# Performance work log

Hardware: AMD Instinct MI355X
Metric: run time of the kernel (lower is better)

The kernel has to match this reference:

```python
import jax, jax.numpy as jnp
import numpy as np

TOP_K = 2
ALPHA = 1.702
LIMIT = 7.0


def setup_inputs() -> dict:
    key = jax.random.key(0)
    ks = jax.random.split(key, 7)
    B, S, H, I, E = 1, 2048, 1024, 1024, 8
    scale = 0.02
    return {
        "hidden_states": jax.random.normal(ks[0], (B, S, H), dtype=jnp.float32),
        "router_w": jax.random.normal(ks[1], (H, E), dtype=jnp.float32) * scale,
        "router_b": jax.random.normal(ks[2], (E,), dtype=jnp.float32) * scale,
        "gate_up_proj": jax.random.normal(ks[3], (E, H, 2 * I), dtype=jnp.float32) * scale,
        "gate_up_bias": jax.random.normal(ks[4], (E, 2 * I), dtype=jnp.float32) * scale,
        "down_proj": jax.random.normal(ks[5], (E, I, H), dtype=jnp.float32) * scale,
        "down_bias": jax.random.normal(ks[6], (E, H), dtype=jnp.float32) * scale,
    }


def reference(hidden_states, router_w, router_b, gate_up_proj, gate_up_bias, down_proj, down_bias):
    # hidden_states: [B, S, H]; gate_up_proj: [E, H, 2I]; down_proj: [E, I, H]
    E = gate_up_proj.shape[0]
    # --- router (GPT-OSS style): top-k logits, softmax over top-k, scatter to E slots ---
    logits = jnp.einsum("bsh,he->bse", hidden_states, router_w) + router_b  # [B,S,E]
    top_vals, top_idx = jax.lax.top_k(logits, TOP_K)                         # [B,S,K]
    topk_weights = jax.nn.softmax(top_vals, axis=-1)                         # [B,S,K]
    onehot = jax.nn.one_hot(top_idx, E, dtype=logits.dtype)                  # [B,S,K,E]
    router_scores = jnp.einsum("bsk,bske->bse", topk_weights, onehot)        # [B,S,E]
    # --- expert compute (dense over the small expert axis; selection via gather below,
    #     which matches the sparsity-masked grouped matmul + all_to_all_combine math) ---
    gu = jnp.einsum("bsh,ehf->bsef", hidden_states, gate_up_proj) + gate_up_bias  # [B,S,E,2I]
    gate = gu[..., 0::2]  # interleaved gate
    up = gu[..., 1::2]    # interleaved up
    gate = jnp.minimum(gate, LIMIT)
    up = jnp.maximum(jnp.minimum(up, LIMIT), -LIMIT)
    glu = gate * jax.nn.sigmoid(gate * ALPHA)
    activated = (up + 1.0) * glu                                             # [B,S,E,I]
    down = jnp.einsum("bsei,eih->bseh", activated, down_proj) + down_bias    # [B,S,E,H]
    # combine: gather each token's K selected expert outputs, weighted sum
    sel = jnp.take_along_axis(down, top_idx[..., None], axis=2)              # [B,S,K,H]
    output = jnp.einsum("bskh,bsk->bsh", sel, topk_weights)                  # [B,S,H]
    return output, router_scores
```

## Files before the change

### kernel.cpp

```cpp
#include <hip/hip_runtime.h>
#include <stdint.h>


#define Sd 2048
#define Hd 1024
#define Id 1024

typedef __bf16 bf16x8 __attribute__((ext_vector_type(8)));
typedef _Float16 f16x8 __attribute__((ext_vector_type(8)));
typedef float f32x4 __attribute__((ext_vector_type(4)));

__device__ __forceinline__ f32x4 mfma_bf16(bf16x8 a, bf16x8 b, f32x4 c) {
  return __builtin_amdgcn_mfma_f32_16x16x32_bf16(a, b, c, 0, 0, 0);
}

__device__ __forceinline__ void gload16(const __bf16* g, __bf16* l) {
  __builtin_amdgcn_global_load_lds(
      (const __attribute__((address_space(1))) unsigned int*)g,
      (__attribute__((address_space(3))) unsigned int*)l, 16, 0, 0);
}

__device__ __forceinline__ unsigned int packbf(float lo, float hi) {
  __bf16 a = (__bf16)lo, b = (__bf16)hi;
  return (unsigned int)__builtin_bit_cast(unsigned short, a) |
         ((unsigned int)__builtin_bit_cast(unsigned short, b) << 16);
}

__global__ __launch_bounds__(256) void k_router(
    const float* __restrict__ x, const float* __restrict__ rw,
    const float* __restrict__ rb, float* __restrict__ scores,
    float* __restrict__ topw, int* __restrict__ eid,
    __bf16* __restrict__ xb) {
  const int lane = threadIdx.x & 63;
  const int t = blockIdx.x * 4 + (threadIdx.x >> 6);
  float acc[8];
#pragma unroll
  for (int e = 0; e < 8; ++e) acc[e] = 0.f;
  const float* xr = x + (size_t)t * Hd;
  unsigned int* xbo = (unsigned int*)(xb + (size_t)t * Hd);
#pragma unroll
  for (int j = 0; j < 8; ++j) {
    int h = j * 128 + lane * 2;
    float2 xv = *(const float2*)(xr + h);
    xbo[h >> 1] = packbf(xv.x, xv.y);
    const float4* wp = (const float4*)(rw + h * 8);
    float4 a0 = wp[0], a1 = wp[1], b0 = wp[2], b1 = wp[3];
    acc[0] += xv.x * a0.x; acc[1] += xv.x * a0.y;
    acc[2] += xv.x * a0.z; acc[3] += xv.x * a0.w;
    acc[4] += xv.x * a1.x; acc[5] += xv.x * a1.y;
    acc[6] += xv.x * a1.z; acc[7] += xv.x * a1.w;
    acc[0] += xv.y * b0.x; acc[1] += xv.y * b0.y;
    acc[2] += xv.y * b0.z; acc[3] += xv.y * b0.w;
    acc[4] += xv.y * b1.x; acc[5] += xv.y * b1.y;
    acc[6] += xv.y * b1.z; acc[7] += xv.y * b1.w;
  }
#pragma unroll
  for (int m = 32; m >= 1; m >>= 1) {
#pragma unroll
    for (int e = 0; e < 8; ++e) acc[e] += __shfl_xor(acc[e], m, 64);
  }
  if (lane == 0) {
    float lg[8];
#pragma unroll
    for (int e = 0; e < 8; ++e) lg[e] = acc[e] + rb[e];
    int i0 = 0; float v0 = lg[0];
#pragma unroll
    for (int e = 1; e < 8; ++e) if (lg[e] > v0) { v0 = lg[e]; i0 = e; }
    int i1 = -1; float v1 = -3.4e38f;
#pragma unroll
    for (int e = 0; e < 8; ++e) if (e != i0 && lg[e] > v1) { v1 = lg[e]; i1 = e; }
    float e1 = __expf(v1 - v0);
    float s = 1.f + e1;
    float w0 = 1.f / s, w1v = e1 / s;
#pragma unroll
    for (int e = 0; e < 8; ++e)
      scores[t * 8 + e] = (e == i0) ? w0 : ((e == i1) ? w1v : 0.f);
    topw[t * 2] = w0;
    topw[t * 2 + 1] = w1v;
    eid[t] = i0 | (i1 << 4);
  }
}

__global__ __launch_bounds__(256) void k_assign(
    const int* __restrict__ eid, int* __restrict__ cnt,
    int* __restrict__ assign, int* __restrict__ tokmap) {
  __shared__ int lcnt[8];
  const int tid = threadIdx.x;
  if (tid < 8) lcnt[tid] = 0;
  __syncthreads();
  for (int t = tid; t < 2048; t += 256) {
    int v = eid[t];
    int i0 = v & 15, i1 = v >> 4;
    int s0 = atomicAdd(&lcnt[i0], 1);
    assign[i0 * 2048 + s0] = t * 2;
    tokmap[t * 2] = (i0 << 11) | s0;
    int s1 = atomicAdd(&lcnt[i1], 1);
    assign[i1 * 2048 + s1] = t * 2 + 1;
    tokmap[t * 2 + 1] = (i1 << 11) | s1;
  }
  __syncthreads();
  if (tid < 8) cnt[tid] = lcnt[tid];
}

__global__ __launch_bounds__(256) void k_gather(
    const __bf16* __restrict__ xb, const int* __restrict__ cnt,
    const int* __restrict__ assign, __bf16* __restrict__ xg) {
  const int u = blockIdx.x;
  int acc = 0, myE = -1, myU0 = 0, nE = 0;
#pragma unroll
  for (int q = 0; q < 8; ++q) {
    int units = ((cnt[q] + 255) >> 8) * 16;
    if (u >= acc && u < acc + units) { myE = q; myU0 = acc; nE = cnt[q]; }
    acc += units;
  }
  if (myE < 0) return;
  const int lane = threadIdx.x & 63;
  const int wv = threadIdx.x >> 6;
  const int row = lane & 15, koff = (lane >> 4) * 8;
  const int slot = (u - myU0) * 16 + row;
  const bool valid = slot < nE;
  int tok = 0;
  if (valid) tok = assign[myE * 2048 + slot] >> 1;
  const __bf16* src = xb + (size_t)tok * Hd + koff;
#pragma unroll
  for (int s = 0; s < 8; ++s) {
    int k32 = wv + 4 * s;
    bf16x8 v;
#pragma unroll
    for (int j = 0; j < 8; ++j) v[j] = (__bf16)0.f;
    if (valid) v = *(const bf16x8*)(src + k32 * 32);
    *(bf16x8*)(xg + (((size_t)u * 32 + k32) * 64 + lane) * 8) = v;
  }
}

__global__ __launch_bounds__(256) void k_pre1(const float* __restrict__ wgu,
                                              __bf16* __restrict__ w1f) {
  const int b = blockIdx.x;
  const int nt = b & 7, kt = (b >> 3) & 15, e = b >> 7;
  __shared__ unsigned int Ls[16][16][34];
  const int tid = threadIdx.x;
  const int w = tid >> 6, lane = tid & 63;
  const float* src = wgu + (size_t)e * (1024 * 2048) +
                     (size_t)(kt * 64 + w * 16) * 2048 + nt * 256;
  const int i0 = lane * 2;
  const int c0 = i0 & 15, u0 = (i0 >> 4) * 2;
  const int c1 = (i0 + 1) & 15, u1 = ((i0 + 1) >> 4) * 2;
#pragma unroll
  for (int rp = 0; rp < 8; ++rp) {
    float4 fa = *(const float4*)(src + (size_t)(rp * 2) * 2048 + lane * 4);
    float4 fb = *(const float4*)(src + (size_t)(rp * 2 + 1) * 2048 + lane * 4);
    int r = w * 8 + rp;
    Ls[u0][c0][r] = packbf(fa.x, fb.x);
    Ls[u0 + 1][c0][r] = packbf(fa.y, fb.y);
    Ls[u1][c1][r] = packbf(fa.z, fb.z);
    Ls[u1 + 1][c1][r] = packbf(fa.w, fb.w);
  }
  __syncthreads();
  const int khi = lane >> 4, c = lane & 15;
#pragma unroll
  for (int uu = 0; uu < 8; ++uu) {
    int ul = w * 8 + uu, vu = ul >> 1, k32l = ul & 1;
    const unsigned int* p = &Ls[vu][c][k32l * 16 + khi * 4];
    uint2 q0 = *(const uint2*)p;
    uint2 q1 = *(const uint2*)(p + 2);
    int itg = nt * 8 + (vu >> 1), vf = vu & 1;
    size_t row = ((size_t)(e * 64 + itg) * 2 + vf) * 32 + (kt * 2 + k32l);
    uint4 o = {q0.x, q0.y, q1.x, q1.y};
    *(uint4*)(w1f + row * 512 + lane * 8) = o;
  }
}

__global__ __launch_bounds__(256) void k_pre2(const float* __restrict__ wdn,
                                              __bf16* __restrict__ w2f) {
  const int b = blockIdx.x;
  const int nt = b & 3, kt = (b >> 2) & 15, e = b >> 6;
  __shared__ unsigned int Ls[16][16][34];
  const int tid = threadIdx.x;
  const int w = tid >> 6, lane = tid & 63;
  const float* src = wdn + (size_t)e * (1024 * 1024) +
                     (size_t)(kt * 64 + w * 16) * 1024 + nt * 256;
#pragma unroll
  for (int rp = 0; rp < 8; ++rp) {
    float4 fa = *(const float4*)(src + (size_t)(rp * 2) * 1024 + lane * 4);
    float4 fb = *(const float4*)(src + (size_t)(rp * 2 + 1) * 1024 + lane * 4);
    int r = w * 8 + rp;
    float va[4] = {fa.x, fa.y, fa.z, fa.w};
    float vb[4] = {fb.x, fb.y, fb.z, fb.w};
#pragma unroll
    for (int q = 0; q < 4; ++q) {
      int cl = lane * 4 + q;
      Ls[cl >> 4][cl & 15][r] = packbf(va[q], vb[q]);
    }
  }
  __syncthreads();
  const int khi = lane >> 4, c = lane & 15;
#pragma unroll
  for (int uu = 0; uu < 8; ++uu) {
    int ul = w * 8 + uu, Fl = ul >> 1, k32l = ul & 1;
    const unsigned int* p = &Ls[Fl][c][k32l * 16 + khi * 4];
    uint2 q0 = *(const uint2*)p;
    uint2 q1 = *(const uint2*)(p + 2);
    size_t row = (size_t)(e * 64 + nt * 16 + Fl) * 32 + (kt * 2 + k32l);
    uint4 o = {q0.x, q0.y, q1.x, q1.y};
    *(uint4*)(w2f + row * 512 + lane * 8) = o;
  }
}

__global__ __launch_bounds__(512, 4) void k_gemm1(
    const __bf16* __restrict__ xg, const __bf16* __restrict__ w1f,
    const float* __restrict__ gub, const int* __restrict__ cnt,
    __bf16* __restrict__ abuf) {
  const int e = blockIdx.x & 7;
  const int it = blockIdx.x >> 3;
  const int n = cnt[e];
  if (n <= 0) return;
  __shared__ __align__(16) __bf16 Bs[2][32][512];
  __shared__ __align__(16) __bf16 Ts[256][16];
  const int tid = threadIdx.x;
  const int lane = tid & 63;
  const int wv = tid >> 6;

  const __bf16* wbase = w1f + (size_t)((e * 64 + it) * 2) * (32 * 512);
  __bf16* bsf = &Bs[0][0][0];
#pragma unroll
  for (int s = 0; s < 8; ++s) {
    int idx = s * 512 + tid;
    gload16(wbase + (size_t)idx * 8, bsf + (size_t)idx * 8);
  }
  const int iCol = it * 16 + (lane & 15);
  const float bg = gub[e * 2048 + 2 * iCol];
  const float bu = gub[e * 2048 + 2 * iCol + 1];
  int eb = 0;
#pragma unroll
  for (int q = 0; q < 8; ++q) eb += (q < e) ? (((cnt[q] + 255) >> 8) << 8) : 0;
  const int u0 = eb >> 4;
  const int nmt = (n + 255) >> 8;

  for (int mt = 0; mt < nmt; ++mt) {
    __syncthreads();
    const __bf16* ap0 =
        xg + ((size_t)(u0 + mt * 16 + 2 * wv) * 32) * 512 + lane * 8;
    const __bf16* ap1 = ap0 + (size_t)32 * 512;
    f32x4 acc[2][2];
#pragma unroll
    for (int a = 0; a < 2; ++a)
#pragma unroll
      for (int b = 0; b < 2; ++b) acc[a][b] = (f32x4){0.f, 0.f, 0.f, 0.f};
    bf16x8 pf[4][2];
#pragma unroll
    for (int d = 0; d < 4; ++d) {
      pf[d][0] = *(const bf16x8*)(ap0 + d * 512);
      pf[d][1] = *(const bf16x8*)(ap1 + d * 512);
    }
#pragma unroll 4
    for (int ks = 0; ks < 28; ++ks) {
      bf16x8 b0 = *(const bf16x8*)&Bs[0][ks][lane * 8];
      bf16x8 b1 = *(const bf16x8*)&Bs[1][ks][lane * 8];
      acc[0][0] = mfma_bf16(pf[ks & 3][0], b0, acc[0][0]);
      acc[0][1] = mfma_bf16(pf[ks & 3][0], b1, acc[0][1]);
      acc[1][0] = mfma_bf16(pf[ks & 3][1], b0, acc[1][0]);
      acc[1][1] = mfma_bf16(pf[ks & 3][1], b1, acc[1][1]);
      pf[ks & 3][0] = *(const bf16x8*)(ap0 + (ks + 4) * 512);
      pf[ks & 3][1] = *(const bf16x8*)(ap1 + (ks + 4) * 512);
    }
#pragma unroll
    for (int ks = 28; ks < 32; ++ks) {
      bf16x8 b0 = *(const bf16x8*)&Bs[0][ks][lane * 8];
      bf16x8 b1 = *(const bf16x8*)&Bs[1][ks][lane * 8];
      acc[0][0] = mfma_bf16(pf[ks & 3][0], b0, acc[0][0]);
      acc[0][1] = mfma_bf16(pf[ks & 3][0], b1, acc[0][1]);
      acc[1][0] = mfma_bf16(pf[ks & 3][1], b0, acc[1][0]);
      acc[1][1] = mfma_bf16(pf[ks & 3][1], b1, acc[1][1]);
    }
#pragma unroll
    for (int mi = 0; mi < 2; ++mi) {
#pragma unroll
      for (int rr = 0; rr < 4; ++rr) {
        int row = wv * 32 + mi * 16 + (lane >> 4) * 4 + rr;
        float g = fminf(acc[mi][0][rr] + bg, 7.f);
        float u = fminf(fmaxf(acc[mi][1][rr] + bu, -7.f), 7.f);
        float sg = 1.f / (1.f + __expf(-1.702f * g));
        Ts[row][lane & 15] = (__bf16)((u + 1.f) * (g * sg));
      }
    }
    __syncthreads();
    {
      int r = tid & 15, hl = (tid >> 4) & 1, sbl = tid >> 5;
      bf16x8 v = *(const bf16x8*)&Ts[sbl * 16 + r][hl * 8];
      size_t o = (((size_t)(u0 + mt * 16 + sbl) * 32) + (it >> 1)) * 512 +
                 ((((it & 1) * 2 + hl) * 16 + r) * 8);
      *(bf16x8*)(abuf + o) = v;
    }
  }
}

__global__ __launch_bounds__(512, 4) void k_gemm2(
    const __bf16* __restrict__ abuf, const __bf16* __restrict__ w2f,
    const float* __restrict__ dnb, const int* __restrict__ cnt,
    const int* __restrict__ assign, const float* __restrict__ topw,
    _Float16* __restrict__ dbuf) {
  const int e = blockIdx.x & 7;
  const int rdec = blockIdx.x >> 3;
  const int ms = rdec & 1;
  const int ht = rdec >> 1;
  const int n = cnt[e];
  if (n <= 0) return;
  __shared__ __align__(16) __bf16 Bs[2][32][512];
  __shared__ float wgt[256];
  const int tid = threadIdx.x;
  const int lane = tid & 63;
  const int wv = tid >> 6;

  const __bf16* wbase = w2f + (size_t)(e * 64 + ht * 2) * (32 * 512);
  __bf16* bsf = &Bs[0][0][0];
#pragma unroll
  for (int s = 0; s < 8; ++s) {
    int idx = s * 512 + tid;
    gload16(wbase + (size_t)idx * 8, bsf + (size_t)idx * 8);
  }
  int eb = 0;
#pragma unroll
  for (int q = 0; q < 8; ++q) eb += (q < e) ? (((cnt[q] + 255) >> 8) << 8) : 0;
  const int u0 = eb >> 4;
  const int nmt = (n + 255) >> 8;

  for (int mt = ms; mt < nmt; mt += 2) {
    __syncthreads();
    if (tid < 256) {
      int slot = mt * 256 + tid;
      int en = (slot < n) ? assign[e * 2048 + slot] : -1;
      wgt[tid] = (en >= 0) ? topw[en] : 0.f;
    }
    __syncthreads();
    const __bf16* ab0 =
        abuf + ((size_t)(u0 + mt * 16 + 2 * wv) * 32) * 512 + lane * 8;
    const __bf16* ab1 = ab0 + (size_t)32 * 512;
    f32x4 acc[2][2];
#pragma unroll
    for (int a = 0; a < 2; ++a)
#pragma unroll
      for (int b = 0; b < 2; ++b) acc[a][b] = (f32x4){0.f, 0.f, 0.f, 0.f};
    bf16x8 pf[4][2];
#pragma unroll
    for (int d = 0; d < 4; ++d) {
      pf[d][0] = *(const bf16x8*)(ab0 + d * 512);
      pf[d][1] = *(const bf16x8*)(ab1 + d * 512);
    }
#pragma unroll 4
    for (int ks = 0; ks < 28; ++ks) {
      bf16x8 b0 = *(const bf16x8*)&Bs[0][ks][lane * 8];
      bf16x8 b1 = *(const bf16x8*)&Bs[1][ks][lane * 8];
      acc[0][0] = mfma_bf16(pf[ks & 3][0], b0, acc[0][0]);
      acc[0][1] = mfma_bf16(pf[ks & 3][0], b1, acc[0][1]);
      acc[1][0] = mfma_bf16(pf[ks & 3][1], b0, acc[1][0]);
      acc[1][1] = mfma_bf16(pf[ks & 3][1], b1, acc[1][1]);
      pf[ks & 3][0] = *(const bf16x8*)(ab0 + (ks + 4) * 512);
      pf[ks & 3][1] = *(const bf16x8*)(ab1 + (ks + 4) * 512);
    }
#pragma unroll
    for (int ks = 28; ks < 32; ++ks) {
      bf16x8 b0 = *(const bf16x8*)&Bs[0][ks][lane * 8];
      bf16x8 b1 = *(const bf16x8*)&Bs[1][ks][lane * 8];
      acc[0][0] = mfma_bf16(pf[ks & 3][0], b0, acc[0][0]);
      acc[0][1] = mfma_bf16(pf[ks & 3][0], b1, acc[0][1]);
      acc[1][0] = mfma_bf16(pf[ks & 3][1], b0, acc[1][0]);
      acc[1][1] = mfma_bf16(pf[ks & 3][1], b1, acc[1][1]);
    }
#pragma unroll
    for (int ni = 0; ni < 2; ++ni) {
      const int nn = ht * 32 + ni * 16 + (lane & 15);
      const float bias = dnb[e * 1024 + nn];
#pragma unroll
      for (int mi = 0; mi < 2; ++mi) {
#pragma unroll
        for (int rr = 0; rr < 4; ++rr) {
          int row = wv * 32 + mi * 16 + (lane >> 4) * 4 + rr;
          int slot = eb + mt * 256 + row;
          dbuf[(size_t)slot * 1024 + nn] =
              (_Float16)(wgt[row] * (acc[mi][ni][rr] + bias));
        }
      }
    }
  }
}

__global__ __launch_bounds__(256) void k_combine(
    const _Float16* __restrict__ dbuf, const int* __restrict__ tokmap,
    const int* __restrict__ cnt, float* __restrict__ out) {
  const int t = blockIdx.x * 4 + (threadIdx.x >> 6);
  const int lane = threadIdx.x & 63;
  int v0 = tokmap[t * 2], v1 = tokmap[t * 2 + 1];
  int e0 = v0 >> 11, e1 = v1 >> 11;
  int b0 = 0, b1 = 0, acc = 0;
#pragma unroll
  for (int q = 0; q < 8; ++q) {
    if (q == e0) b0 = acc;
    if (q == e1) b1 = acc;
    acc += ((cnt[q] + 255) >> 8) << 8;
  }
  const _Float16* r0 = dbuf + (size_t)(b0 + (v0 & 2047)) * 1024 + lane * 16;
  const _Float16* r1 = dbuf + (size_t)(b1 + (v1 & 2047)) * 1024 + lane * 16;
  float* o = out + (size_t)t * 1024 + lane * 16;
#pragma unroll
  for (int h = 0; h < 2; ++h) {
    f16x8 a = *(const f16x8*)(r0 + h * 8);
    f16x8 b = *(const f16x8*)(r1 + h * 8);
    float4 o0, o1;
    o0.x = (float)a[0] + (float)b[0];
    o0.y = (float)a[1] + (float)b[1];
    o0.z = (float)a[2] + (float)b[2];
    o0.w = (float)a[3] + (float)b[3];
    o1.x = (float)a[4] + (float)b[4];
    o1.y = (float)a[5] + (float)b[5];
    o1.z = (float)a[6] + (float)b[6];
    o1.w = (float)a[7] + (float)b[7];
    *(float4*)(o + h * 8) = o0;
    *(float4*)(o + h * 8 + 4) = o1;
  }
}

extern "C" void kernel_launch(void* const* d_in, const int* in_sizes, int n_in,
                              void* d_out, int out_size, void* d_ws, size_t ws_size,
                              hipStream_t stream) {
  const float* x   = (const float*)d_in[0];
  const float* rw  = (const float*)d_in[1];
  const float* rb  = (const float*)d_in[2];
  const float* wgu = (const float*)d_in[3];
  const float* gub = (const float*)d_in[4];
  const float* wdn = (const float*)d_in[5];
  const float* dnb = (const float*)d_in[6];
  float* out = (float*)d_out;
  float* scores = out + (size_t)Sd * Hd;

  char* ws = (char*)d_ws;
  int* cnt     = (int*)ws;
  int* assign  = (int*)(ws + 256);
  float* topw  = (float*)(ws + 256 + 65536);
  int* tokmap  = (int*)(ws + 256 + 65536 + 16384);
  int* eid     = (int*)(ws + 256 + 65536 + 32768);
  __bf16* xg   = (__bf16*)(ws + ((size_t)1 << 20));
  __bf16* abuf = (__bf16*)(ws + ((size_t)15 << 20));
  __bf16* xb   = (__bf16*)(ws + ((size_t)28 << 20));
  __bf16* w1f  = (__bf16*)(ws + ((size_t)28 << 20));
  __bf16* w2f  = (__bf16*)(ws + ((size_t)28 << 20));
  _Float16* dbuf = (_Float16*)(ws + ((size_t)44 << 20));

  k_router<<<512, 256, 0, stream>>>(x, rw, rb, scores, topw, eid, xb);
  k_assign<<<1, 256, 0, stream>>>(eid, cnt, assign, tokmap);
  k_gather<<<384, 256, 0, stream>>>(xb, cnt, assign, xg);
  k_pre1<<<1024, 256, 0, stream>>>(wgu, w1f);
  k_gemm1<<<512, 512, 0, stream>>>(xg, w1f, gub, cnt, abuf);
  k_pre2<<<512, 256, 0, stream>>>(wdn, w2f);
  k_gemm2<<<512, 512, 0, stream>>>(abuf, w2f, dnb, cnt, assign, topw, dbuf);
  k_combine<<<512, 256, 0, stream>>>(dbuf, tokmap, cnt, out);
}
```

Baseline: 117.8 us.

## Split M-tiles across more blocks and halve LDS weight tiles in expert GEMMs

Both expert GEMM kernels launch twice as many blocks, each handling a strided subset of M-tiles. The weight tile held in shared memory shrinks to 16 K-steps, with the second half reloaded mid-loop behind extra barriers, and launch bounds rise to allow 6 blocks per CU. The aim is more parallelism and occupancy for the small per-expert workloads. In exchange, weights are reloaded from global/L2 for every M-tile, and each tile pays extra synchronisation and load latency.

After: 132.9 us. +12.8%, slower.

```diff
diff --git a/kernel.cpp b/kernel.cpp
--- a/kernel.cpp
+++ b/kernel.cpp
@@ -206,27 +206,23 @@
   }
 }
 
-__global__ __launch_bounds__(512, 4) void k_gemm1(
+__global__ __launch_bounds__(512, 6) void k_gemm1(
     const __bf16* __restrict__ xg, const __bf16* __restrict__ w1f,
     const float* __restrict__ gub, const int* __restrict__ cnt,
     __bf16* __restrict__ abuf) {
   const int e = blockIdx.x & 7;
-  const int it = blockIdx.x >> 3;
+  const int r = blockIdx.x >> 3;
+  const int it = r & 63;
+  const int ms = r >> 6;
   const int n = cnt[e];
   if (n <= 0) return;
-  __shared__ __align__(16) __bf16 Bs[2][32][512];
+  __shared__ __align__(16) __bf16 Bs[2][16][512];
   __shared__ __align__(16) __bf16 Ts[256][16];
   const int tid = threadIdx.x;
   const int lane = tid & 63;
   const int wv = tid >> 6;
 
   const __bf16* wbase = w1f + (size_t)((e * 64 + it) * 2) * (32 * 512);
-  __bf16* bsf = &Bs[0][0][0];
-#pragma unroll
-  for (int s = 0; s < 8; ++s) {
-    int idx = s * 512 + tid;
-    gload16(wbase + (size_t)idx * 8, bsf + (size_t)idx * 8);
-  }
   const int iCol = it * 16 + (lane & 15);
   const float bg = gub[e * 2048 + 2 * iCol];
   const float bu = gub[e * 2048 + 2 * iCol + 1];
@@ -236,8 +232,14 @@
   const int u0 = eb >> 4;
   const int nmt = (n + 255) >> 8;
 
-  for (int mt = 0; mt < nmt; ++mt) {
+  for (int mt = ms; mt < nmt; mt += 2) {
     __syncthreads();
+#pragma unroll
+    for (int s = 0; s < 4; ++s) {
+      int idx = s * 512 + tid;
+      int vf = idx >> 10, k = (idx >> 6) & 15, l = idx & 63;
+      gload16(wbase + (size_t)(vf * 32 + k) * 512 + l * 8, &Bs[vf][k][l * 8]);
+    }
     const __bf16* ap0 =
         xg + ((size_t)(u0 + mt * 16 + 2 * wv) * 32) * 512 + lane * 8;
     const __bf16* ap1 = ap0 + (size_t)32 * 512;
@@ -246,31 +248,47 @@
     for (int a = 0; a < 2; ++a)
 #pragma unroll
       for (int b = 0; b < 2; ++b) acc[a][b] = (f32x4){0.f, 0.f, 0.f, 0.f};
-    bf16x8 pf[4][2];
-#pragma unroll
-    for (int d = 0; d < 4; ++d) {
-      pf[d][0] = *(const bf16x8*)(ap0 + d * 512);
-      pf[d][1] = *(const bf16x8*)(ap1 + d * 512);
-    }
+    __syncthreads();
+#pragma unroll
+    for (int seg = 0; seg < 2; ++seg) {
+      const int kb = seg * 16;
+      bf16x8 pf[4][2];
+#pragma unroll
+      for (int d = 0; d < 4; ++d) {
+        pf[d][0] = *(const bf16x8*)(ap0 + (kb + d) * 512);
+        pf[d][1] = *(const bf16x8*)(ap1 + (kb + d) * 512);
+      }
 #pragma unroll 4
-    for (int ks = 0; ks < 28; ++ks) {
-      bf16x8 b0 = *(const bf16x8*)&Bs[0][ks][lane * 8];
-      bf16x8 b1 = *(const bf16x8*)&Bs[1][ks][lane * 8];
-      acc[0][0] = mfma_bf16(pf[ks & 3][0], b0, acc[0][0]);
-      acc[0][1] = mfma_bf16(pf[ks & 3][0], b1, acc[0][1]);
-      acc[1][0] = mfma_bf16(pf[ks & 3][1], b0, acc[1][0]);
-      acc[1][1] = mfma_bf16(pf[ks & 3][1], b1, acc[1][1]);
-      pf[ks & 3][0] = *(const bf16x8*)(ap0 + (ks + 4) * 512);
-      pf[ks & 3][1] = *(const bf16x8*)(ap1 + (ks + 4) * 512);
-    }
-#pragma unroll
-    for (int ks = 28; ks < 32; ++ks) {
-      bf16x8 b0 = *(const bf16x8*)&Bs[0][ks][lane * 8];
-      bf16x8 b1 = *(const bf16x8*)&Bs[1][ks][lane * 8];
-      acc[0][0] = mfma_bf16(pf[ks & 3][0], b0, acc[0][0]);
-      acc[0][1] = mfma_bf16(pf[ks & 3][0], b1, acc[0][1]);
-      acc[1][0] = mfma_bf16(pf[ks & 3][1], b0, acc[1][0]);
-      acc[1][1] = mfma_bf16(pf[ks & 3][1], b1, acc[1][1]);
+      for (int j = 0; j < 12; ++j) {
+        bf16x8 b0 = *(const bf16x8*)&Bs[0][j][lane * 8];
+        bf16x8 b1 = *(const bf16x8*)&Bs[1][j][lane * 8];
+        acc[0][0] = mfma_bf16(pf[j & 3][0], b0, acc[0][0]);
+        acc[0][1] = mfma_bf16(pf[j & 3][0], b1, acc[0][1]);
+        acc[1][0] = mfma_bf16(pf[j & 3][1], b0, acc[1][0]);
+        acc[1][1] = mfma_bf16(pf[j & 3][1], b1, acc[1][1]);
+        pf[j & 3][0] = *(const bf16x8*)(ap0 + (kb + j + 4) * 512);
+        pf[j & 3][1] = *(const bf16x8*)(ap1 + (kb + j + 4) * 512);
+      }
+#pragma unroll
+      for (int j = 12; j < 16; ++j) {
+        bf16x8 b0 = *(const bf16x8*)&Bs[0][j][lane * 8];
+        bf16x8 b1 = *(const bf16x8*)&Bs[1][j][lane * 8];
+        acc[0][0] = mfma_bf16(pf[j & 3][0], b0, acc[0][0]);
+        acc[0][1] = mfma_bf16(pf[j & 3][0], b1, acc[0][1]);
+        acc[1][0] = mfma_bf16(pf[j & 3][1], b0, acc[1][0]);
+        acc[1][1] = mfma_bf16(pf[j & 3][1], b1, acc[1][1]);
+      }
+      if (seg == 0) {
+        __syncthreads();
+#pragma unroll
+        for (int s = 0; s < 4; ++s) {
+          int idx = s * 512 + tid;
+          int vf = idx >> 10, k = (idx >> 6) & 15, l = idx & 63;
+          gload16(wbase + (size_t)(vf * 32 + 16 + k) * 512 + l * 8,
+                  &Bs[vf][k][l * 8]);
+        }
+        __syncthreads();
+      }
     }
 #pragma unroll
     for (int mi = 0; mi < 2; ++mi) {
@@ -285,53 +303,52 @@
     }
     __syncthreads();
     {
-      int r = tid & 15, hl = (tid >> 4) & 1, sbl = tid >> 5;
-      bf16x8 v = *(const bf16x8*)&Ts[sbl * 16 + r][hl * 8];
+      int rrow = tid & 15, hl = (tid >> 4) & 1, sbl = tid >> 5;
+      bf16x8 v = *(const bf16x8*)&Ts[sbl * 16 + rrow][hl * 8];
       size_t o = (((size_t)(u0 + mt * 16 + sbl) * 32) + (it >> 1)) * 512 +
-                 ((((it & 1) * 2 + hl) * 16 + r) * 8);
+                 ((((it & 1) * 2 + hl) * 16 + rrow) * 8);
       *(bf16x8*)(abuf + o) = v;
     }
   }
 }
 
-__global__ __launch_bounds__(512, 4) void k_gemm2(
+__global__ __launch_bounds__(512, 6) void k_gemm2(
     const __bf16* __restrict__ abuf, const __bf16* __restrict__ w2f,
     const float* __restrict__ dnb, const int* __restrict__ cnt,
     const int* __restrict__ assign, const float* __restrict__ topw,
     _Float16* __restrict__ dbuf) {
   const int e = blockIdx.x & 7;
-  const int rdec = blockIdx.x >> 3;
-  const int ms = rdec & 1;
-  const int ht = rdec >> 1;
+  const int r = blockIdx.x >> 3;
+  const int ht = r & 31;
+  const int ms = r >> 5;
   const int n = cnt[e];
   if (n <= 0) return;
-  __shared__ __align__(16) __bf16 Bs[2][32][512];
+  __shared__ __align__(16) __bf16 Bs[2][16][512];
   __shared__ float wgt[256];
   const int tid = threadIdx.x;
   const int lane = tid & 63;
   const int wv = tid >> 6;
 
   const __bf16* wbase = w2f + (size_t)(e * 64 + ht * 2) * (32 * 512);
-  __bf16* bsf = &Bs[0][0][0];
-#pragma unroll
-  for (int s = 0; s < 8; ++s) {
-    int idx = s * 512 + tid;
-    gload16(wbase + (size_t)idx * 8, bsf + (size_t)idx * 8);
-  }
   int eb = 0;
 #pragma unroll
   for (int q = 0; q < 8; ++q) eb += (q < e) ? (((cnt[q] + 255) >> 8) << 8) : 0;
   const int u0 = eb >> 4;
   const int nmt = (n + 255) >> 8;
 
-  for (int mt = ms; mt < nmt; mt += 2) {
+  for (int mt = ms; mt < nmt; mt += 4) {
     __syncthreads();
     if (tid < 256) {
       int slot = mt * 256 + tid;
       int en = (slot < n) ? assign[e * 2048 + slot] : -1;
       wgt[tid] = (en >= 0) ? topw[en] : 0.f;
     }
-    __syncthreads();
+#pragma unroll
+    for (int s = 0; s < 4; ++s) {
+      int idx = s * 512 + tid;
+      int nf = idx >> 10, k = (idx >> 6) & 15, l = idx & 63;
+      gload16(wbase + (size_t)(nf * 32 + k) * 512 + l * 8, &Bs[nf][k][l * 8]);
+    }
     const __bf16* ab0 =
         abuf + ((size_t)(u0 + mt * 16 + 2 * wv) * 32) * 512 + lane * 8;
     const __bf16* ab1 = ab0 + (size_t)32 * 512;
@@ -340,31 +357,47 @@
     for (int a = 0; a < 2; ++a)
 #pragma unroll
       for (int b = 0; b < 2; ++b) acc[a][b] = (f32x4){0.f, 0.f, 0.f, 0.f};
-    bf16x8 pf[4][2];
-#pragma unroll
-    for (int d = 0; d < 4; ++d) {
-      pf[d][0] = *(const bf16x8*)(ab0 + d * 512);
-      pf[d][1] = *(const bf16x8*)(ab1 + d * 512);
-    }
+    __syncthreads();
+#pragma unroll
+    for (int seg = 0; seg < 2; ++seg) {
+      const int kb = seg * 16;
+      bf16x8 pf[4][2];
+#pragma unroll
+      for (int d = 0; d < 4; ++d) {
+        pf[d][0] = *(const bf16x8*)(ab0 + (kb + d) * 512);
+        pf[d][1] = *(const bf16x8*)(ab1 + (kb + d) * 512);
+      }
 #pragma unroll 4
-    for (int ks = 0; ks < 28; ++ks) {
-      bf16x8 b0 = *(const bf16x8*)&Bs[0][ks][lane * 8];
-      bf16x8 b1 = *(const bf16x8*)&Bs[1][ks][lane * 8];
-      acc[0][0] = mfma_bf16(pf[ks & 3][0], b0, acc[0][0]);
-      acc[0][1] = mfma_bf16(pf[ks & 3][0], b1, acc[0][1]);
-      acc[1][0] = mfma_bf16(pf[ks & 3][1], b0, acc[1][0]);
-      acc[1][1] = mfma_bf16(pf[ks & 3][1], b1, acc[1][1]);
-      pf[ks & 3][0] = *(const bf16x8*)(ab0 + (ks + 4) * 512);
-      pf[ks & 3][1] = *(const bf16x8*)(ab1 + (ks + 4) * 512);
-    }
-#pragma unroll
-    for (int ks = 28; ks < 32; ++ks) {
-      bf16x8 b0 = *(const bf16x8*)&Bs[0][ks][lane * 8];
-      bf16x8 b1 = *(const bf16x8*)&Bs[1][ks][lane * 8];
-      acc[0][0] = mfma_bf16(pf[ks & 3][0], b0, acc[0][0]);
-      acc[0][1] = mfma_bf16(pf[ks & 3][0], b1, acc[0][1]);
-      acc[1][0] = mfma_bf16(pf[ks & 3][1], b0, acc[1][0]);
-      acc[1][1] = mfma_bf16(pf[ks & 3][1], b1, acc[1][1]);
+      for (int j = 0; j < 12; ++j) {
+        bf16x8 b0 = *(const bf16x8*)&Bs[0][j][lane * 8];
+        bf16x8 b1 = *(const bf16x8*)&Bs[1][j][lane * 8];
+        acc[0][0] = mfma_bf16(pf[j & 3][0], b0, acc[0][0]);
+        acc[0][1] = mfma_bf16(pf[j & 3][0], b1, acc[0][1]);
+        acc[1][0] = mfma_bf16(pf[j & 3][1], b0, acc[1][0]);
+        acc[1][1] = mfma_bf16(pf[j & 3][1], b1, acc[1][1]);
+        pf[j & 3][0] = *(const bf16x8*)(ab0 + (kb + j + 4) * 512);
+        pf[j & 3][1] = *(const bf16x8*)(ab1 + (kb + j + 4) * 512);
+      }
+#pragma unroll
+      for (int j = 12; j < 16; ++j) {
+        bf16x8 b0 = *(const bf16x8*)&Bs[0][j][lane * 8];
+        bf16x8 b1 = *(const bf16x8*)&Bs[1][j][lane * 8];
+        acc[0][0] = mfma_bf16(pf[j & 3][0], b0, acc[0][0]);
+        acc[0][1] = mfma_bf16(pf[j & 3][0], b1, acc[0][1]);
+        acc[1][0] = mfma_bf16(pf[j & 3][1], b0, acc[1][0]);
+        acc[1][1] = mfma_bf16(pf[j & 3][1], b1, acc[1][1]);
+      }
+      if (seg == 0) {
+        __syncthreads();
+#pragma unroll
+        for (int s = 0; s < 4; ++s) {
+          int idx = s * 512 + tid;
+          int nf = idx >> 10, k = (idx >> 6) & 15, l = idx & 63;
+          gload16(wbase + (size_t)(nf * 32 + 16 + k) * 512 + l * 8,
+                  &Bs[nf][k][l * 8]);
+        }
+        __syncthreads();
+      }
     }
 #pragma unroll
     for (int ni = 0; ni < 2; ++ni) {
@@ -449,8 +482,8 @@
   k_assign<<<1, 256, 0, stream>>>(eid, cnt, assign, tokmap);
   k_gather<<<384, 256, 0, stream>>>(xb, cnt, assign, xg);
   k_pre1<<<1024, 256, 0, stream>>>(wgu, w1f);
-  k_gemm1<<<512, 512, 0, stream>>>(xg, w1f, gub, cnt, abuf);
+  k_gemm1<<<1024, 512, 0, stream>>>(xg, w1f, gub, cnt, abuf);
   k_pre2<<<512, 256, 0, stream>>>(wdn, w2f);
-  k_gemm2<<<512, 512, 0, stream>>>(abuf, w2f, dnb, cnt, assign, topw, dbuf);
+  k_gemm2<<<1024, 512, 0, stream>>>(abuf, w2f, dnb, cnt, assign, topw, dbuf);
   k_combine<<<512, 256, 0, stream>>>(dbuf, tokmap, cnt, out);
 }
```

## Widen GEMM N-tiles to four weight panels per block in both expert GEMMs

Applied to the files above, without the earlier changes.

Each block in both expert GEMMs now stages four 32x512 weight panels in LDS instead of two. Every activation fragment loaded from global memory therefore feeds eight MFMAs instead of four. To keep the grid size unchanged, the M-tile loop is strided across blocks: two ways in gemm1 and four ways in gemm2. The gemm1 epilogue writes a full 32-column activation row segment. The LDS footprint grows to about 128KB per block, which limits residency to one block per CU. That loss of latency hiding may offset the better reuse of activation loads.

Result: faster. 114.2 us (median of 2 runs) (-3.1%).

```diff
diff --git a/kernel.cpp b/kernel.cpp
--- a/kernel.cpp
+++ b/kernel.cpp
@@ -206,46 +206,52 @@
   }
 }
 
-__global__ __launch_bounds__(512, 4) void k_gemm1(
+__global__ __launch_bounds__(512, 2) void k_gemm1(
     const __bf16* __restrict__ xg, const __bf16* __restrict__ w1f,
     const float* __restrict__ gub, const int* __restrict__ cnt,
     __bf16* __restrict__ abuf) {
   const int e = blockIdx.x & 7;
-  const int it = blockIdx.x >> 3;
+  const int r = blockIdx.x >> 3;
+  const int it = r & 31;
+  const int ms = r >> 5;
   const int n = cnt[e];
   if (n <= 0) return;
-  __shared__ __align__(16) __bf16 Bs[2][32][512];
-  __shared__ __align__(16) __bf16 Ts[256][16];
+  __shared__ __align__(16) __bf16 Bs[4][32][512];
+  __shared__ __align__(16) __bf16 Ts[256][48];
   const int tid = threadIdx.x;
   const int lane = tid & 63;
   const int wv = tid >> 6;
 
-  const __bf16* wbase = w1f + (size_t)((e * 64 + it) * 2) * (32 * 512);
-  __bf16* bsf = &Bs[0][0][0];
-#pragma unroll
-  for (int s = 0; s < 8; ++s) {
+#pragma unroll
+  for (int s = 0; s < 16; ++s) {
     int idx = s * 512 + tid;
-    gload16(wbase + (size_t)idx * 8, bsf + (size_t)idx * 8);
-  }
-  const int iCol = it * 16 + (lane & 15);
-  const float bg = gub[e * 2048 + 2 * iCol];
-  const float bu = gub[e * 2048 + 2 * iCol + 1];
+    int v = idx >> 11, k = (idx >> 6) & 31, l = idx & 63;
+    size_t rowv = (size_t)(e * 64 + it * 2 + (v >> 1)) * 2 + (v & 1);
+    gload16(w1f + (rowv * 32 + k) * 512 + l * 8, &Bs[v][k][l * 8]);
+  }
+  float bgv[2], buv[2];
+#pragma unroll
+  for (int p = 0; p < 2; ++p) {
+    const int col = it * 32 + p * 16 + (lane & 15);
+    bgv[p] = gub[e * 2048 + 2 * col];
+    buv[p] = gub[e * 2048 + 2 * col + 1];
+  }
   int eb = 0;
 #pragma unroll
   for (int q = 0; q < 8; ++q) eb += (q < e) ? (((cnt[q] + 255) >> 8) << 8) : 0;
   const int u0 = eb >> 4;
   const int nmt = (n + 255) >> 8;
 
-  for (int mt = 0; mt < nmt; ++mt) {
+  for (int mt = ms; mt < nmt; mt += 2) {
     __syncthreads();
     const __bf16* ap0 =
         xg + ((size_t)(u0 + mt * 16 + 2 * wv) * 32) * 512 + lane * 8;
     const __bf16* ap1 = ap0 + (size_t)32 * 512;
-    f32x4 acc[2][2];
+    f32x4 acc[2][4];
 #pragma unroll
     for (int a = 0; a < 2; ++a)
 #pragma unroll
-      for (int b = 0; b < 2; ++b) acc[a][b] = (f32x4){0.f, 0.f, 0.f, 0.f};
+      for (int b = 0; b < 4; ++b) acc[a][b] = (f32x4){0.f, 0.f, 0.f, 0.f};
     bf16x8 pf[4][2];
 #pragma unroll
     for (int d = 0; d < 4; ++d) {
@@ -254,69 +260,80 @@
     }
 #pragma unroll 4
     for (int ks = 0; ks < 28; ++ks) {
-      bf16x8 b0 = *(const bf16x8*)&Bs[0][ks][lane * 8];
-      bf16x8 b1 = *(const bf16x8*)&Bs[1][ks][lane * 8];
-      acc[0][0] = mfma_bf16(pf[ks & 3][0], b0, acc[0][0]);
-      acc[0][1] = mfma_bf16(pf[ks & 3][0], b1, acc[0][1]);
-      acc[1][0] = mfma_bf16(pf[ks & 3][1], b0, acc[1][0]);
-      acc[1][1] = mfma_bf16(pf[ks & 3][1], b1, acc[1][1]);
+      bf16x8 b[4];
+#pragma unroll
+      for (int v = 0; v < 4; ++v) b[v] = *(const bf16x8*)&Bs[v][ks][lane * 8];
+#pragma unroll
+      for (int v = 0; v < 4; ++v) {
+        acc[0][v] = mfma_bf16(pf[ks & 3][0], b[v], acc[0][v]);
+        acc[1][v] = mfma_bf16(pf[ks & 3][1], b[v], acc[1][v]);
+      }
       pf[ks & 3][0] = *(const bf16x8*)(ap0 + (ks + 4) * 512);
       pf[ks & 3][1] = *(const bf16x8*)(ap1 + (ks + 4) * 512);
     }
 #pragma unroll
     for (int ks = 28; ks < 32; ++ks) {
-      bf16x8 b0 = *(const bf16x8*)&Bs[0][ks][lane * 8];
-      bf16x8 b1 = *(const bf16x8*)&Bs[1][ks][lane * 8];
-      acc[0][0] = mfma_bf16(pf[ks & 3][0], b0, acc[0][0]);
-      acc[0][1] = mfma_bf16(pf[ks & 3][0], b1, acc[0][1]);
-      acc[1][0] = mfma_bf16(pf[ks & 3][1], b0, acc[1][0]);
-      acc[1][1] = mfma_bf16(pf[ks & 3][1], b1, acc[1][1]);
-    }
-#pragma unroll
-    for (int mi = 0; mi < 2; ++mi) {
-#pragma unroll
-      for (int rr = 0; rr < 4; ++rr) {
-        int row = wv * 32 + mi * 16 + (lane >> 4) * 4 + rr;
-        float g = fminf(acc[mi][0][rr] + bg, 7.f);
-        float u = fminf(fmaxf(acc[mi][1][rr] + bu, -7.f), 7.f);
-        float sg = 1.f / (1.f + __expf(-1.702f * g));
-        Ts[row][lane & 15] = (__bf16)((u + 1.f) * (g * sg));
+      bf16x8 b[4];
+#pragma unroll
+      for (int v = 0; v < 4; ++v) b[v] = *(const bf16x8*)&Bs[v][ks][lane * 8];
+#pragma unroll
+      for (int v = 0; v < 4; ++v) {
+        acc[0][v] = mfma_bf16(pf[ks & 3][0], b[v], acc[0][v]);
+        acc[1][v] = mfma_bf16(pf[ks & 3][1], b[v], acc[1][v]);
+      }
+    }
+#pragma unroll
+    for (int itgl = 0; itgl < 2; ++itgl) {
+      const int colL = itgl * 16 + (lane & 15);
+#pragma unroll
+      for (int mi = 0; mi < 2; ++mi) {
+        f32x4 ag = acc[mi][itgl * 2];
+        f32x4 au = acc[mi][itgl * 2 + 1];
+#pragma unroll
+        for (int rr = 0; rr < 4; ++rr) {
+          int row = wv * 32 + mi * 16 + (lane >> 4) * 4 + rr;
+          float g = fminf(ag[rr] + bgv[itgl], 7.f);
+          float u = fminf(fmaxf(au[rr] + buv[itgl], -7.f), 7.f);
+          float sg = 1.f / (1.f + __expf(-1.702f * g));
+          Ts[row][colL] = (__bf16)((u + 1.f) * (g * sg));
+        }
       }
     }
     __syncthreads();
-    {
-      int r = tid & 15, hl = (tid >> 4) & 1, sbl = tid >> 5;
-      bf16x8 v = *(const bf16x8*)&Ts[sbl * 16 + r][hl * 8];
-      size_t o = (((size_t)(u0 + mt * 16 + sbl) * 32) + (it >> 1)) * 512 +
-                 ((((it & 1) * 2 + hl) * 16 + r) * 8);
+#pragma unroll
+    for (int h2 = 0; h2 < 2; ++h2) {
+      int idx = h2 * 512 + tid;
+      int sbl = idx >> 6, l = idx & 63;
+      bf16x8 v = *(const bf16x8*)&Ts[sbl * 16 + (l & 15)][(l >> 4) * 8];
+      size_t o = ((size_t)(u0 + mt * 16 + sbl) * 32 + it) * 512 + l * 8;
       *(bf16x8*)(abuf + o) = v;
     }
   }
 }
 
-__global__ __launch_bounds__(512, 4) void k_gemm2(
+__global__ __launch_bounds__(512, 2) void k_gemm2(
     const __bf16* __restrict__ abuf, const __bf16* __restrict__ w2f,
     const float* __restrict__ dnb, const int* __restrict__ cnt,
     const int* __restrict__ assign, const float* __restrict__ topw,
     _Float16* __restrict__ dbuf) {
   const int e = blockIdx.x & 7;
-  const int rdec = blockIdx.x >> 3;
-  const int ms = rdec & 1;
-  const int ht = rdec >> 1;
+  const int r = blockIdx.x >> 3;
+  const int ht = r & 15;
+  const int ms = r >> 4;
   const int n = cnt[e];
   if (n <= 0) return;
-  __shared__ __align__(16) __bf16 Bs[2][32][512];
+  __shared__ __align__(16) __bf16 Bs[4][32][512];
   __shared__ float wgt[256];
   const int tid = threadIdx.x;
   const int lane = tid & 63;
   const int wv = tid >> 6;
 
-  const __bf16* wbase = w2f + (size_t)(e * 64 + ht * 2) * (32 * 512);
-  __bf16* bsf = &Bs[0][0][0];
-#pragma unroll
-  for (int s = 0; s < 8; ++s) {
+#pragma unroll
+  for (int s = 0; s < 16; ++s) {
     int idx = s * 512 + tid;
-    gload16(wbase + (size_t)idx * 8, bsf + (size_t)idx * 8);
+    int v = idx >> 11, k = (idx >> 6) & 31, l = idx & 63;
+    size_t rowv = (size_t)(e * 64 + ht * 4 + v);
+    gload16(w2f + (rowv * 32 + k) * 512 + l * 8, &Bs[v][k][l * 8]);
   }
   int eb = 0;
 #pragma unroll
@@ -324,7 +341,7 @@
   const int u0 = eb >> 4;
   const int nmt = (n + 255) >> 8;
 
-  for (int mt = ms; mt < nmt; mt += 2) {
+  for (int mt = ms; mt < nmt; mt += 4) {
     __syncthreads();
     if (tid < 256) {
       int slot = mt * 256 + tid;
@@ -335,11 +352,11 @@
     const __bf16* ab0 =
         abuf + ((size_t)(u0 + mt * 16 + 2 * wv) * 32) * 512 + lane * 8;
     const __bf16* ab1 = ab0 + (size_t)32 * 512;
-    f32x4 acc[2][2];
+    f32x4 acc[2][4];
 #pragma unroll
     for (int a = 0; a < 2; ++a)
 #pragma unroll
-      for (int b = 0; b < 2; ++b) acc[a][b] = (f32x4){0.f, 0.f, 0.f, 0.f};
+      for (int b = 0; b < 4; ++b) acc[a][b] = (f32x4){0.f, 0.f, 0.f, 0.f};
     bf16x8 pf[4][2];
 #pragma unroll
     for (int d = 0; d < 4; ++d) {
@@ -348,27 +365,31 @@
     }
 #pragma unroll 4
     for (int ks = 0; ks < 28; ++ks) {
-      bf16x8 b0 = *(const bf16x8*)&Bs[0][ks][lane * 8];
-      bf16x8 b1 = *(const bf16x8*)&Bs[1][ks][lane * 8];
-      acc[0][0] = mfma_bf16(pf[ks & 3][0], b0, acc[0][0]);
-      acc[0][1] = mfma_bf16(pf[ks & 3][0], b1, acc[0][1]);
-      acc[1][0] = mfma_bf16(pf[ks & 3][1], b0, acc[1][0]);
-      acc[1][1] = mfma_bf16(pf[ks & 3][1], b1, acc[1][1]);
+      bf16x8 b[4];
+#pragma unroll
+      for (int v = 0; v < 4; ++v) b[v] = *(const bf16x8*)&Bs[v][ks][lane * 8];
+#pragma unroll
+      for (int v = 0; v < 4; ++v) {
+        acc[0][v] = mfma_bf16(pf[ks & 3][0], b[v], acc[0][v]);
+        acc[1][v] = mfma_bf16(pf[ks & 3][1], b[v], acc[1][v]);
+      }
       pf[ks & 3][0] = *(const bf16x8*)(ab0 + (ks + 4) * 512);
       pf[ks & 3][1] = *(const bf16x8*)(ab1 + (ks + 4) * 512);
     }
 #pragma unroll
     for (int ks = 28; ks < 32; ++ks) {
-      bf16x8 b0 = *(const bf16x8*)&Bs[0][ks][lane * 8];
-      bf16x8 b1 = *(const bf16x8*)&Bs[1][ks][lane * 8];
-      acc[0][0] = mfma_bf16(pf[ks & 3][0], b0, acc[0][0]);
-      acc[0][1] = mfma_bf16(pf[ks & 3][0], b1, acc[0][1]);
-      acc[1][0] = mfma_bf16(pf[ks & 3][1], b0, acc[1][0]);
-      acc[1][1] = mfma_bf16(pf[ks & 3][1], b1, acc[1][1]);
-    }
-#pragma unroll
-    for (int ni = 0; ni < 2; ++ni) {
-      const int nn = ht * 32 + ni * 16 + (lane & 15);
+      bf16x8 b[4];
+#pragma unroll
+      for (int v = 0; v < 4; ++v) b[v] = *(const bf16x8*)&Bs[v][ks][lane * 8];
+#pragma unroll
+      for (int v = 0; v < 4; ++v) {
+        acc[0][v] = mfma_bf16(pf[ks & 3][0], b[v], acc[0][v]);
+        acc[1][v] = mfma_bf16(pf[ks & 3][1], b[v], acc[1][v]);
+      }
+    }
+#pragma unroll
+    for (int v = 0; v < 4; ++v) {
+      const int nn = ht * 64 + v * 16 + (lane & 15);
       const float bias = dnb[e * 1024 + nn];
 #pragma unroll
       for (int mi = 0; mi < 2; ++mi) {
@@ -377,7 +398,7 @@
           int row = wv * 32 + mi * 16 + (lane >> 4) * 4 + rr;
           int slot = eb + mt * 256 + row;
           dbuf[(size_t)slot * 1024 + nn] =
-              (_Float16)(wgt[row] * (acc[mi][ni][rr] + bias));
+              (_Float16)(wgt[row] * (acc[mi][v][rr] + bias));
         }
       }
     }
```
